# Performance work log

Hardware: AMD Instinct MI355X
Metric: run time of the kernel (lower is better)

Reference implementation:

```python
import jax, jax.numpy as jnp
import numpy as np

B, ORDER, N, D, H = 16, 2, 512, 128, 8
DH = D // H
NEG_SLOPE = 0.2


def setup_inputs() -> dict:
    key = jax.random.key(0)
    ks = jax.random.split(key, 8)
    stdv = 1.0 / np.sqrt(DH)

    def u(k, shape):
        return jax.random.uniform(k, shape, jnp.float32, -stdv, stdv)

    x = jax.random.normal(ks[0], (B, ORDER, N, D), jnp.float32)
    A = jax.random.randint(ks[1], (B, ORDER, N, N), 0, 5, jnp.int32)
    # Stacked params for the 2*order GAT modules: axis0 = order, axis1 = (conv1, conv2)
    W = u(ks[2], (ORDER, 2, D, D))            # project.weight
    pb = jnp.zeros((ORDER, 2, D), jnp.float32)  # project.bias (init 0)
    att_src = u(ks[3], (ORDER, 2, H, DH))
    att_dst = u(ks[4], (ORDER, 2, H, DH))
    bias = jnp.zeros((ORDER, 2, D), jnp.float32)  # GAT output bias (init 0)
    return {"x": x, "A": A, "W": W, "pb": pb,
            "att_src": att_src, "att_dst": att_dst, "bias": bias}


def _gat(x, Af, W, pb, a_src, a_dst, b):
    # x: [B,N,D]; Af: [B,N,N] float in {0,1}
    xp = x @ W.T + pb                                  # project
    xh = xp.reshape(B, N, H, DH)                       # [B,N,H,DH]
    s_src = jnp.einsum('bnhd,hd->bnh', xh, a_src)      # [B,N,H]
    s_dst = jnp.einsum('bnhd,hd->bnh', xh, a_dst)
    alpha = s_src[:, :, None, :] + s_dst[:, None, :, :]  # [B,src,dst,H]
    alpha = jnp.where((Af != 1.0)[..., None], 0.0, alpha)
    alpha = jnp.where(alpha >= 0, alpha, NEG_SLOPE * alpha)  # leaky relu
    alpha = jax.nn.softmax(alpha, axis=1)              # softmax over src dim
    out = jnp.einsum('bsdh,bshf->bdhf', alpha, xh).reshape(B, N, D)
    out = out + xp                                     # add_self_loops
    return out + b


def reference(x, A, W, pb, att_src, att_dst, bias):
    A1 = ((A == 2) | (A == 4)).astype(x.dtype)  # [B,ORDER,N,N]
    A2 = ((A == 3) | (A == 4)).astype(x.dtype)
    hs = []
    for i in range(ORDER):
        h1 = _gat(x[:, i], A1[:, i], W[i, 0], pb[i, 0], att_src[i, 0], att_dst[i, 0], bias[i, 0])
        h2 = _gat(x[:, i], A2[:, i], W[i, 1], pb[i, 1], att_src[i, 1], att_dst[i, 1], bias[i, 1])
        hs.append(h1 + h2)
    h = jnp.stack(hs, axis=1)                          # [B,ORDER,N,D]
    out = h + h.mean(axis=1, keepdims=True)
    return out
```

## Files before the change

### kernel.cpp

```cpp
#include <hip/hip_runtime.h>

#define N_ 512
#define D_ 128
#define LOG2E 1.44269504088896f


typedef __attribute__((ext_vector_type(8))) short short8;
typedef __attribute__((ext_vector_type(4))) float floatx4;
typedef __attribute__((ext_vector_type(4))) unsigned int uintx4;
typedef __attribute__((ext_vector_type(2))) _Float16 half2v;
typedef __attribute__((ext_vector_type(8))) _Float16 half8;

#if defined(__has_builtin)
#if __has_builtin(__builtin_amdgcn_exp2f)
#define EXP2F(x) __builtin_amdgcn_exp2f(x)
#else
#define EXP2F(x) exp2f(x)
#endif
#else
#define EXP2F(x) exp2f(x)
#endif

__device__ __forceinline__ unsigned int pkh(float a, float b) {
    auto h = __builtin_amdgcn_cvt_pkrtz(a, b);
    return __builtin_bit_cast(unsigned int, h);
}

__global__ __launch_bounds__(256) void prep_kernel(
    const float* __restrict__ x, const float* __restrict__ W,
    const float* __restrict__ pb, const float* __restrict__ att_src,
    const float* __restrict__ att_dst, const int* __restrict__ A,
    unsigned short* __restrict__ xpt, unsigned int* __restrict__ sgEs,
    unsigned int* __restrict__ sgFs, float2* __restrict__ sgD,
    unsigned int* __restrict__ mgT)
{
    const int bid0 = blockIdx.x;
    const int t = threadIdx.x;

    if (bid0 >= 1024) {
        const int bid = bid0 - 1024;
        const int bi = bid >> 4;
        const int rem = bid & 15;
        const int dg = rem >> 2;
        const int jw = rem & 3;
        const int dp = t & 63, q = t >> 6;
        const int dstb = dg * 128 + dp * 2;
        const int sbase = jw * 128 + q * 8;
        const int* Ab = A + (size_t)bi * N_ * N_ + dstb;
        unsigned int a00 = 0, a01 = 0, a10 = 0, a11 = 0;
#pragma unroll
        for (int cp = 0; cp < 4; ++cp) {
#pragma unroll
            for (int i = 0; i < 8; ++i) {
                const int s = sbase + cp * 32 + i;
                const int2 v = *(const int2*)(Ab + (size_t)s * N_);
                const int bitp = cp * 8 + i;
                a00 |= ((0x14u >> v.x) & 1u) << bitp;
                a10 |= ((0x18u >> v.x) & 1u) << bitp;
                a01 |= ((0x14u >> v.y) & 1u) << bitp;
                a11 |= ((0x18u >> v.y) & 1u) << bitp;
            }
        }
        const int i0 = bi * 2;
        mgT[(((size_t)i0 * 4 + q) * 512 + dstb + 0) * 4 + jw] = a00;
        mgT[(((size_t)i0 * 4 + q) * 512 + dstb + 1) * 4 + jw] = a01;
        mgT[(((size_t)(i0 + 1) * 4 + q) * 512 + dstb + 0) * 4 + jw] = a10;
        mgT[(((size_t)(i0 + 1) * 4 + q) * 512 + dstb + 1) * 4 + jw] = a11;
        return;
    }

    const int unit = bid0 >> 1;
    const int half = bid0 & 1;
    const int ntile = unit & 7;
    const int inst  = unit >> 3;
    const int j = inst & 1;
    const int bi = inst >> 1;
    const int ij = (bi & 1) * 2 + j;
    const int wave = t >> 6, L = t & 63, n = L & 15, q = L >> 4;

    const int n0w = ntile * 64 + wave * 16;
    const float* xrow = x + ((size_t)bi * N_ + n0w + n) * D_ + q * 8;
    half8 Af[4];
#pragma unroll
    for (int kc = 0; kc < 4; ++kc) {
        const float4 a0 = *(const float4*)(xrow + kc * 32);
        const float4 a1 = *(const float4*)(xrow + kc * 32 + 4);
        uintx4 au;
        au.x = pkh(a0.x, a0.y);
        au.y = pkh(a0.z, a0.w);
        au.z = pkh(a1.x, a1.y);
        au.w = pkh(a1.z, a1.w);
        Af[kc] = __builtin_bit_cast(half8, au);
    }

    const float* wb = W + (size_t)ij * D_ * D_;
#pragma unroll
    for (int ft = 0; ft < 4; ++ft) {
        const int head = half * 4 + ft;
        const int fg = head * 16 + n;
        const float* wrow = wb + (size_t)fg * D_ + q * 8;
        floatx4 C = (floatx4){0.f, 0.f, 0.f, 0.f};
#pragma unroll
        for (int kc = 0; kc < 4; ++kc) {
            const float4 b0 = *(const float4*)(wrow + kc * 32);
            const float4 b1 = *(const float4*)(wrow + kc * 32 + 4);
            uintx4 bu;
            bu.x = pkh(b0.x, b0.y);
            bu.y = pkh(b0.z, b0.w);
            bu.z = pkh(b1.x, b1.y);
            bu.w = pkh(b1.z, b1.w);
            C = __builtin_amdgcn_mfma_f32_16x16x32_f16(
                Af[kc], __builtin_bit_cast(half8, bu), C, 0, 0, 0);
        }
        const float pbv = pb[ij * D_ + fg];
        float xp0 = C[0] + pbv, xp1 = C[1] + pbv;
        float xp2 = C[2] + pbv, xp3 = C[3] + pbv;
        uint2 pk;
        pk.x = pkh(xp0, xp1);
        pk.y = pkh(xp2, xp3);
        *(uint2*)&xpt[((size_t)inst * D_ + fg) * N_ + n0w + q * 4] = pk;

        const float asv = att_src[ij * D_ + fg];
        const float adv = att_dst[ij * D_ + fg];
        float sa0 = xp0 * asv, sa1 = xp1 * asv, sa2 = xp2 * asv, sa3 = xp3 * asv;
        float sb0 = xp0 * adv, sb1 = xp1 * adv, sb2 = xp2 * adv, sb3 = xp3 * adv;
#pragma unroll
        for (int off = 1; off < 16; off <<= 1) {
            sa0 += __shfl_xor(sa0, off); sa1 += __shfl_xor(sa1, off);
            sa2 += __shfl_xor(sa2, off); sa3 += __shfl_xor(sa3, off);
            sb0 += __shfl_xor(sb0, off); sb1 += __shfl_xor(sb1, off);
            sb2 += __shfl_xor(sb2, off); sb3 += __shfl_xor(sb3, off);
        }
        if (n < 4) {
            const float vlo = ((n & 1) ? sa2 : sa0) * LOG2E;
            const float vhi = ((n & 1) ? sa3 : sa1) * LOG2E;
            const float sc = (n < 2) ? 1.0f : 0.2f;
            const unsigned int pkv = pkh(EXP2F(sc * vlo), EXP2F(sc * vhi));
            unsigned int* dstp = (n < 2) ? sgEs : sgFs;
            dstp[((size_t)inst * 8 + head) * 256 + (n0w >> 1) + q * 2 + (n & 1)] = pkv;
        } else if (n >= 8 && n < 12) {
            const int r = n - 8;
            const float v = ((r == 0) ? sb0 : (r == 1) ? sb1 : (r == 2) ? sb2 : sb3) * LOG2E;
            float2 ed;
            ed.x = EXP2F(v);
            ed.y = EXP2F(0.2f * v);
            sgD[((size_t)inst * 8 + head) * N_ + n0w + q * 4 + r] = ed;
        }
    }
}

__global__ __launch_bounds__(256) void attn_kernel(
    const unsigned short* __restrict__ xpt,
    const unsigned int* __restrict__ sgEs,
    const unsigned int* __restrict__ sgFs,
    const float2* __restrict__ sgD,
    const unsigned int* __restrict__ mgT,
    const float* __restrict__ bias,
    float* __restrict__ hout)
{
    __shared__ unsigned int es_l[8 * 256];
    __shared__ unsigned int fs_l[8 * 256];
    __shared__ unsigned int seltab[4];

    const int bid = blockIdx.x;
    const int tile = bid & 31;
    const int cj   = (bid >> 5) & 1;
    const int bi   = bid >> 6;
    const int inst = bi * 2 + cj;
    const int ij = (bi & 1) * 2 + cj;
    const int d0 = tile * 16;
    const int t = threadIdx.x;
    const int wave = t >> 6, L = t & 63, n = L & 15, q = L >> 4;
    const int h0 = wave * 2;

    {
        const uint4* sE = (const uint4*)(sgEs + (size_t)inst * 2048);
        const uint4* sF = (const uint4*)(sgFs + (size_t)inst * 2048);
        ((uint4*)es_l)[t]       = sE[t];
        ((uint4*)es_l)[256 + t] = sE[256 + t];
        ((uint4*)fs_l)[t]       = sF[t];
        ((uint4*)fs_l)[256 + t] = sF[256 + t];
    }
    if (t < 4) seltab[t] = ((t & 1) ? 0x0000FFFFu : 0u) | ((t & 2) ? 0xFFFF0000u : 0u);

    const uint4 mreg = *(const uint4*)(mgT + (((size_t)inst * 4 + q) * 512 + d0 + n) * 4);
    const unsigned int mw_[4] = { mreg.x, mreg.y, mreg.z, mreg.w };

    unsigned int iEd2[2], rd2[2];
#pragma unroll
    for (int hh = 0; hh < 2; ++hh) {
        const float2 ed = sgD[((size_t)inst * 8 + h0 + hh) * N_ + d0 + n];
        const float iEd = 1.0f / ed.x;
        const float rdv = ed.y * iEd;
        iEd2[hh] = pkh(iEd, iEd);
        rd2[hh] = pkh(rdv, rdv);
    }

    __syncthreads();

    const unsigned short* xpi = xpt + (size_t)inst * D_ * N_;
    const unsigned short* bp0 = xpi + (size_t)(h0 * 16 + n) * N_;
    const unsigned short* bp1 = xpi + (size_t)((h0 + 1) * 16 + n) * N_;

    const uintx4 ou = { 0x3C003C00u, 0x3C003C00u, 0x3C003C00u, 0x3C003C00u };
    const half8 onesB = __builtin_bit_cast(half8, ou);

    floatx4 Cacc[2] = { (floatx4){0.f,0.f,0.f,0.f}, (floatx4){0.f,0.f,0.f,0.f} };
    floatx4 Cz[2]   = { (floatx4){0.f,0.f,0.f,0.f}, (floatx4){0.f,0.f,0.f,0.f} };

    uintx4 B0 = *(const uintx4*)(bp0 + q * 8);
    uintx4 B1 = *(const uintx4*)(bp1 + q * 8);
#pragma unroll
    for (int c = 0; c < 16; ++c) {
        const int sq = c * 32 + q * 8;
        uintx4 nB0, nB1;
        if (c < 15) {
            nB0 = *(const uintx4*)(bp0 + sq + 32);
            nB1 = *(const uintx4*)(bp1 + sq + 32);
        }
        const unsigned int word = mw_[c >> 2];
        unsigned int sel[4];
#pragma unroll
        for (int p = 0; p < 4; ++p) {
            const int sh = (c & 3) * 8 + 2 * p;
            const unsigned int b4 = (sh >= 2) ? ((word >> (sh - 2)) & 12u)
                                              : ((word << 2) & 12u);
            sel[p] = *(const unsigned int*)((const char*)seltab + b4);
        }
        const int spb = c * 16 + q * 4;
#pragma unroll
        for (int hh = 0; hh < 2; ++hh) {
            const uint4 Ep = *(const uint4*)&es_l[(h0 + hh) * 256 + spb];
            const uint4 Fp = *(const uint4*)&fs_l[(h0 + hh) * 256 + spb];
            const unsigned int eu[4] = { Ep.x, Ep.y, Ep.z, Ep.w };
            const unsigned int fu[4] = { Fp.x, Fp.y, Fp.z, Fp.w };
            const half2v rdh = __builtin_bit_cast(half2v, rd2[hh]);
            uintx4 au;
            unsigned int wts[4];
#pragma unroll
            for (int p = 0; p < 4; ++p) {
                const half2v e = __builtin_bit_cast(half2v, eu[p]);
                const half2v f = __builtin_bit_cast(half2v, fu[p]);
                const half2v pr = f * rdh;
                const half2v wv = __builtin_elementwise_max(pr, e);
                const unsigned int wvu = __builtin_bit_cast(unsigned int, wv);
                wts[p] = (sel[p] & wvu) | (~sel[p] & iEd2[hh]);
            }
            au.x = wts[0]; au.y = wts[1]; au.z = wts[2]; au.w = wts[3];
            const half8 As = __builtin_bit_cast(half8, au);
            Cacc[hh] = __builtin_amdgcn_mfma_f32_16x16x32_f16(
                As, __builtin_bit_cast(half8, hh ? B1 : B0), Cacc[hh], 0, 0, 0);
            Cz[hh] = __builtin_amdgcn_mfma_f32_16x16x32_f16(
                As, onesB, Cz[hh], 0, 0, 0);
        }
        B0 = nB0;
        B1 = nB1;
    }

#pragma unroll
    for (int hh = 0; hh < 2; ++hh) {
        const int h = h0 + hh;
        const float bv = bias[ij * D_ + h * 16 + n];
        const uint2 sv = *(const uint2*)(xpi + (size_t)(h * 16 + n) * N_ + d0 + q * 4);
        const half2v s0 = __builtin_bit_cast(half2v, sv.x);
        const half2v s1 = __builtin_bit_cast(half2v, sv.y);
        const float selfv[4] = { (float)s0[0], (float)s0[1],
                                 (float)s1[0], (float)s1[1] };
#pragma unroll
        for (int reg = 0; reg < 4; ++reg) {
            const float Zi = 1.0f / Cz[hh][reg];
            const float val = Cacc[hh][reg] * Zi + selfv[reg] + bv;
            unsafeAtomicAdd(
                &hout[((size_t)bi * N_ + d0 + q * 4 + reg) * D_ + h * 16 + n], val);
        }
    }
}

__global__ __launch_bounds__(256) void combine_kernel(float* __restrict__ h)
{
    const int idx = blockIdx.x * 256 + threadIdx.x;
    const int b = idx >> 14;
    const int r = idx & 16383;
    float4* p0 = (float4*)h + (size_t)b * 32768 + r;
    float4* p1 = p0 + 16384;
    const float4 a = *p0;
    const float4 o = *p1;
    float4 r0, r1;
    r0.x = 1.5f * a.x + 0.5f * o.x;  r1.x = 1.5f * o.x + 0.5f * a.x;
    r0.y = 1.5f * a.y + 0.5f * o.y;  r1.y = 1.5f * o.y + 0.5f * a.y;
    r0.z = 1.5f * a.z + 0.5f * o.z;  r1.z = 1.5f * o.z + 0.5f * a.z;
    r0.w = 1.5f * a.w + 0.5f * o.w;  r1.w = 1.5f * o.w + 0.5f * a.w;
    *p0 = r0;
    *p1 = r1;
}

extern "C" void kernel_launch(void* const* d_in, const int* in_sizes, int n_in,
                              void* d_out, int out_size, void* d_ws, size_t ws_size,
                              hipStream_t stream)
{
    const float* x   = (const float*)d_in[0];
    const int*   A   = (const int*)d_in[1];
    const float* W   = (const float*)d_in[2];
    const float* pb  = (const float*)d_in[3];
    const float* as_ = (const float*)d_in[4];
    const float* ad_ = (const float*)d_in[5];
    const float* bs  = (const float*)d_in[6];

    unsigned short* xpt = (unsigned short*)d_ws;
    unsigned int* sgEs = (unsigned int*)((char*)d_ws + (8u << 20));
    unsigned int* sgFs = (unsigned int*)((char*)d_ws + (8u << 20) + (512u << 10));
    float2* sgD = (float2*)((char*)d_ws + (9u << 20));
    unsigned int* mgT = (unsigned int*)((char*)d_ws + (11u << 20));
    float* h = (float*)d_out;

    (void)hipMemsetAsync(d_out, 0, (size_t)out_size * sizeof(float), stream);
    prep_kernel<<<1536, 256, 0, stream>>>(x, W, pb, as_, ad_, A, xpt, sgEs, sgFs, sgD, mgT);
    attn_kernel<<<2048, 256, 0, stream>>>(xpt, sgEs, sgFs, sgD, mgT, bs, h);
    combine_kernel<<<1024, 256, 0, stream>>>(h);
}
```

Baseline: 152.5 us.

## Fold attention vectors into W for scores; merge both convs per attn block

The prep kernel now computes W^T·att vectors once per block in shared memory and gets the source and destination scores with one extra MFMA, instead of shuffle-reducing the projected features per head. The attention kernel now runs both GAT convs for a tile in one 512-thread block and sums them through shared memory with plain stores. This removes the atomics and the output memset. The cost is lower precision in the fp16 folded score vectors, a larger block, and extra block syncs.

```diff
diff --git a/kernel.cpp b/kernel.cpp
--- a/kernel.cpp
+++ b/kernel.cpp
@@ -34,6 +34,9 @@
     unsigned int* __restrict__ sgFs, float2* __restrict__ sgD,
     unsigned int* __restrict__ mgT)
 {
+    __shared__ _Float16 va_l[8][136];
+    __shared__ float c0_l[8];
+
     const int bid0 = blockIdx.x;
     const int t = threadIdx.x;
 
@@ -77,6 +80,35 @@
     const int bi = inst >> 1;
     const int ij = (bi & 1) * 2 + j;
     const int wave = t >> 6, L = t & 63, n = L & 15, q = L >> 4;
+    const float* wb = W + (size_t)ij * D_ * D_;
+
+    {
+        const int c = t >> 5;
+        const int k0 = (t & 31) * 4;
+        const int hn = half * 4 + (c & 3);
+        const float* av = ((c < 4) ? att_src : att_dst) + ij * D_ + hn * 16;
+        const float* Wh = wb + (size_t)(hn * 16) * D_ + k0;
+        float a0 = 0.f, a1 = 0.f, a2 = 0.f, a3 = 0.f;
+#pragma unroll
+        for (int dd = 0; dd < 16; ++dd) {
+            const float a = av[dd];
+            const float4 wv = *(const float4*)(Wh + (size_t)dd * D_);
+            a0 += wv.x * a; a1 += wv.y * a; a2 += wv.z * a; a3 += wv.w * a;
+        }
+        va_l[c][k0 + 0] = (_Float16)(a0 * LOG2E);
+        va_l[c][k0 + 1] = (_Float16)(a1 * LOG2E);
+        va_l[c][k0 + 2] = (_Float16)(a2 * LOG2E);
+        va_l[c][k0 + 3] = (_Float16)(a3 * LOG2E);
+        if (t < 8) {
+            const int hn2 = half * 4 + (t & 3);
+            const float* av2 = ((t < 4) ? att_src : att_dst) + ij * D_ + hn2 * 16;
+            const float* pbp = pb + ij * D_ + hn2 * 16;
+            float s = 0.f;
+#pragma unroll
+            for (int dd = 0; dd < 16; ++dd) s += pbp[dd] * av2[dd];
+            c0_l[t] = s * LOG2E;
+        }
+    }
 
     const int n0w = ntile * 64 + wave * 16;
     const float* xrow = x + ((size_t)bi * N_ + n0w + n) * D_ + q * 8;
@@ -93,7 +125,18 @@
         Af[kc] = __builtin_bit_cast(half8, au);
     }
 
-    const float* wb = W + (size_t)ij * D_ * D_;
+    __syncthreads();
+
+    floatx4 S = (floatx4){0.f, 0.f, 0.f, 0.f};
+    {
+        const _Float16* var = &va_l[n & 7][q * 8];
+#pragma unroll
+        for (int kc = 0; kc < 4; ++kc) {
+            const half8 Bs = *(const half8*)(var + kc * 32);
+            S = __builtin_amdgcn_mfma_f32_16x16x32_f16(Af[kc], Bs, S, 0, 0, 0);
+        }
+    }
+
 #pragma unroll
     for (int ft = 0; ft < 4; ++ft) {
         const int head = half * 4 + ft;
@@ -113,43 +156,35 @@
                 Af[kc], __builtin_bit_cast(half8, bu), C, 0, 0, 0);
         }
         const float pbv = pb[ij * D_ + fg];
-        float xp0 = C[0] + pbv, xp1 = C[1] + pbv;
-        float xp2 = C[2] + pbv, xp3 = C[3] + pbv;
         uint2 pk;
-        pk.x = pkh(xp0, xp1);
-        pk.y = pkh(xp2, xp3);
+        pk.x = pkh(C[0] + pbv, C[1] + pbv);
+        pk.y = pkh(C[2] + pbv, C[3] + pbv);
         *(uint2*)&xpt[((size_t)inst * D_ + fg) * N_ + n0w + q * 4] = pk;
-
-        const float asv = att_src[ij * D_ + fg];
-        const float adv = att_dst[ij * D_ + fg];
-        float sa0 = xp0 * asv, sa1 = xp1 * asv, sa2 = xp2 * asv, sa3 = xp3 * asv;
-        float sb0 = xp0 * adv, sb1 = xp1 * adv, sb2 = xp2 * adv, sb3 = xp3 * adv;
-#pragma unroll
-        for (int off = 1; off < 16; off <<= 1) {
-            sa0 += __shfl_xor(sa0, off); sa1 += __shfl_xor(sa1, off);
-            sa2 += __shfl_xor(sa2, off); sa3 += __shfl_xor(sa3, off);
-            sb0 += __shfl_xor(sb0, off); sb1 += __shfl_xor(sb1, off);
-            sb2 += __shfl_xor(sb2, off); sb3 += __shfl_xor(sb3, off);
-        }
+    }
+
+    if (n < 8) {
+        const float cc = c0_l[n];
+        const float v0 = S[0] + cc, v1 = S[1] + cc;
+        const float v2 = S[2] + cc, v3 = S[3] + cc;
         if (n < 4) {
-            const float vlo = ((n & 1) ? sa2 : sa0) * LOG2E;
-            const float vhi = ((n & 1) ? sa3 : sa1) * LOG2E;
-            const float sc = (n < 2) ? 1.0f : 0.2f;
-            const unsigned int pkv = pkh(EXP2F(sc * vlo), EXP2F(sc * vhi));
-            unsigned int* dstp = (n < 2) ? sgEs : sgFs;
-            dstp[((size_t)inst * 8 + head) * 256 + (n0w >> 1) + q * 2 + (n & 1)] = pkv;
-        } else if (n >= 8 && n < 12) {
-            const int r = n - 8;
-            const float v = ((r == 0) ? sb0 : (r == 1) ? sb1 : (r == 2) ? sb2 : sb3) * LOG2E;
-            float2 ed;
-            ed.x = EXP2F(v);
-            ed.y = EXP2F(0.2f * v);
-            sgD[((size_t)inst * 8 + head) * N_ + n0w + q * 4 + r] = ed;
-        }
-    }
-}
-
-__global__ __launch_bounds__(256) void attn_kernel(
+            const int head = half * 4 + n;
+            const size_t base = ((size_t)inst * 8 + head) * 256 + (n0w >> 1) + q * 2;
+            sgEs[base + 0] = pkh(EXP2F(v0), EXP2F(v1));
+            sgEs[base + 1] = pkh(EXP2F(v2), EXP2F(v3));
+            sgFs[base + 0] = pkh(EXP2F(0.2f * v0), EXP2F(0.2f * v1));
+            sgFs[base + 1] = pkh(EXP2F(0.2f * v2), EXP2F(0.2f * v3));
+        } else {
+            const int head = half * 4 + (n - 4);
+            const size_t base = ((size_t)inst * 8 + head) * N_ + n0w + q * 4;
+            float2 e0; e0.x = EXP2F(v0); e0.y = EXP2F(0.2f * v0); sgD[base + 0] = e0;
+            float2 e1; e1.x = EXP2F(v1); e1.y = EXP2F(0.2f * v1); sgD[base + 1] = e1;
+            float2 e2; e2.x = EXP2F(v2); e2.y = EXP2F(0.2f * v2); sgD[base + 2] = e2;
+            float2 e3; e3.x = EXP2F(v3); e3.y = EXP2F(0.2f * v3); sgD[base + 3] = e3;
+        }
+    }
+}
+
+__global__ __launch_bounds__(512, 8) void attn_kernel(
     const unsigned short* __restrict__ xpt,
     const unsigned int* __restrict__ sgEs,
     const unsigned int* __restrict__ sgFs,
@@ -158,28 +193,28 @@
     const float* __restrict__ bias,
     float* __restrict__ hout)
 {
-    __shared__ unsigned int es_l[8 * 256];
-    __shared__ unsigned int fs_l[8 * 256];
+    __shared__ unsigned int smem[8192];
     __shared__ unsigned int seltab[4];
 
     const int bid = blockIdx.x;
     const int tile = bid & 31;
-    const int cj   = (bid >> 5) & 1;
-    const int bi   = bid >> 6;
-    const int inst = bi * 2 + cj;
-    const int ij = (bi & 1) * 2 + cj;
+    const int bi   = bid >> 5;
+    const int i0   = bi * 2;
     const int d0 = tile * 16;
     const int t = threadIdx.x;
     const int wave = t >> 6, L = t & 63, n = L & 15, q = L >> 4;
-    const int h0 = wave * 2;
+    const int cv = wave >> 2;
+    const int h0 = (wave & 3) * 2;
+    const int inst = i0 + cv;
+    const int ij = (bi & 1) * 2 + cv;
 
     {
-        const uint4* sE = (const uint4*)(sgEs + (size_t)inst * 2048);
-        const uint4* sF = (const uint4*)(sgFs + (size_t)inst * 2048);
-        ((uint4*)es_l)[t]       = sE[t];
-        ((uint4*)es_l)[256 + t] = sE[256 + t];
-        ((uint4*)fs_l)[t]       = sF[t];
-        ((uint4*)fs_l)[256 + t] = sF[256 + t];
+        const uint4* sE = (const uint4*)(sgEs + (size_t)i0 * 2048);
+        const uint4* sF = (const uint4*)(sgFs + (size_t)i0 * 2048);
+        uint4* dE = (uint4*)smem;
+        uint4* dF = (uint4*)(smem + 4096);
+        dE[t] = sE[t]; dE[512 + t] = sE[512 + t];
+        dF[t] = sF[t]; dF[512 + t] = sF[512 + t];
     }
     if (t < 4) seltab[t] = ((t & 1) ? 0x0000FFFFu : 0u) | ((t & 2) ? 0xFFFF0000u : 0u);
 
@@ -201,6 +236,8 @@
     const unsigned short* xpi = xpt + (size_t)inst * D_ * N_;
     const unsigned short* bp0 = xpi + (size_t)(h0 * 16 + n) * N_;
     const unsigned short* bp1 = xpi + (size_t)((h0 + 1) * 16 + n) * N_;
+    const unsigned int* esw = smem + cv * 2048;
+    const unsigned int* fsw = smem + 4096 + cv * 2048;
 
     const uintx4 ou = { 0x3C003C00u, 0x3C003C00u, 0x3C003C00u, 0x3C003C00u };
     const half8 onesB = __builtin_bit_cast(half8, ou);
@@ -230,8 +267,8 @@
         const int spb = c * 16 + q * 4;
 #pragma unroll
         for (int hh = 0; hh < 2; ++hh) {
-            const uint4 Ep = *(const uint4*)&es_l[(h0 + hh) * 256 + spb];
-            const uint4 Fp = *(const uint4*)&fs_l[(h0 + hh) * 256 + spb];
+            const uint4 Ep = *(const uint4*)&esw[(h0 + hh) * 256 + spb];
+            const uint4 Fp = *(const uint4*)&fsw[(h0 + hh) * 256 + spb];
             const unsigned int eu[4] = { Ep.x, Ep.y, Ep.z, Ep.w };
             const unsigned int fu[4] = { Fp.x, Fp.y, Fp.z, Fp.w };
             const half2v rdh = __builtin_bit_cast(half2v, rd2[hh]);
@@ -257,6 +294,7 @@
         B1 = nB1;
     }
 
+    float vals[2][4];
 #pragma unroll
     for (int hh = 0; hh < 2; ++hh) {
         const int h = h0 + hh;
@@ -269,10 +307,27 @@
 #pragma unroll
         for (int reg = 0; reg < 4; ++reg) {
             const float Zi = 1.0f / Cz[hh][reg];
-            const float val = Cacc[hh][reg] * Zi + selfv[reg] + bv;
-            unsafeAtomicAdd(
-                &hout[((size_t)bi * N_ + d0 + q * 4 + reg) * D_ + h * 16 + n], val);
-        }
+            vals[hh][reg] = Cacc[hh][reg] * Zi + selfv[reg] + bv;
+        }
+    }
+
+    __syncthreads();
+    float* out_l = (float*)smem;
+    if (cv == 1) {
+#pragma unroll
+        for (int hh = 0; hh < 2; ++hh)
+#pragma unroll
+            for (int reg = 0; reg < 4; ++reg)
+                out_l[(q * 4 + reg) * 132 + (h0 + hh) * 16 + n] = vals[hh][reg];
+    }
+    __syncthreads();
+    if (cv == 0) {
+#pragma unroll
+        for (int hh = 0; hh < 2; ++hh)
+#pragma unroll
+            for (int reg = 0; reg < 4; ++reg)
+                hout[((size_t)bi * N_ + d0 + q * 4 + reg) * D_ + (h0 + hh) * 16 + n] =
+                    vals[hh][reg] + out_l[(q * 4 + reg) * 132 + (h0 + hh) * 16 + n];
     }
 }
 
@@ -313,8 +368,7 @@
     unsigned int* mgT = (unsigned int*)((char*)d_ws + (11u << 20));
     float* h = (float*)d_out;
 
-    (void)hipMemsetAsync(d_out, 0, (size_t)out_size * sizeof(float), stream);
     prep_kernel<<<1536, 256, 0, stream>>>(x, W, pb, as_, ad_, A, xpt, sgEs, sgFs, sgD, mgT);
-    attn_kernel<<<2048, 256, 0, stream>>>(xpt, sgEs, sgFs, sgD, mgT, bs, h);
+    attn_kernel<<<1024, 512, 0, stream>>>(xpt, sgEs, sgFs, sgD, mgT, bs, h);
     combine_kernel<<<1024, 256, 0, stream>>>(h);
 }
```

Measured after the change: 153.0 us. No clear change (+0.3%).
